# Kernel optimization log

Measured on AMD Instinct MI355X. Metric: run time of the kernel, lower is better.

## Reference

```python
import jax, jax.numpy as jnp
import numpy as np

B, T_ENC, D_IN = 64, 32, 4096
T_DEC, D_WORD = 20, 300
H = 512
VOCAB = 20000


def lstm_scan(x_tbd, W, b, c0, h0):
    """TF BasicLSTMCell (forget_bias=1.0, gate order i,j,f,o) scanned over time.
    x_tbd: [T,B,D]; W: [D+H, 4H]; returns (c,h) final state and all h [T,B,H]."""
    def step(carry, x):
        c, h = carry
        z = jnp.concatenate([x, h], axis=-1) @ W + b  # [B,4H]
        i, j, f, o = jnp.split(z, 4, axis=-1)
        c = c * jax.nn.sigmoid(f + 1.0) + jax.nn.sigmoid(i) * jnp.tanh(j)
        h = jnp.tanh(c) * jax.nn.sigmoid(o)
        return (c, h), h
    (c, h), hs = jax.lax.scan(step, (c0, h0), x_tbd)
    return (c, h), hs


def setup_inputs() -> dict:
    key = jax.random.key(0)
    ks = jax.random.split(key, 8)
    frames = jax.random.normal(ks[0], (B, T_ENC, D_IN), dtype=jnp.float32)
    caption = jax.random.randint(ks[1], (B, T_DEC), 0, VOCAB, dtype=jnp.int32)
    embeddings = jax.random.normal(ks[2], (VOCAB, D_WORD), dtype=jnp.float32) * 0.1
    s_enc = 1.0 / np.sqrt(D_IN + H)
    s_dec = 1.0 / np.sqrt(D_WORD + H)
    W_enc = jax.random.normal(ks[3], (D_IN + H, 4 * H), dtype=jnp.float32) * s_enc
    b_enc = jnp.zeros((4 * H,), dtype=jnp.float32)
    W_dec = jax.random.normal(ks[4], (D_WORD + H, 4 * H), dtype=jnp.float32) * s_dec
    b_dec = jnp.zeros((4 * H,), dtype=jnp.float32)
    W_proj = jax.random.normal(ks[5], (H, D_WORD), dtype=jnp.float32) / np.sqrt(H)
    b_proj = jnp.zeros((D_WORD,), dtype=jnp.float32)
    return {"frames": frames, "embeddings": embeddings, "W_enc": W_enc,
            "b_enc": b_enc, "W_dec": W_dec, "b_dec": b_dec,
            "W_proj": W_proj, "b_proj": b_proj, "caption": caption}


def reference(frames, embeddings, W_enc, b_enc, W_dec, b_dec, W_proj, b_proj, caption):
    b = frames.shape[0]
    c0 = jnp.zeros((b, H), dtype=frames.dtype)
    h0 = jnp.zeros((b, H), dtype=frames.dtype)
    # encoder over frames (dropout keep_prob=1 -> identity)
    (c, h), _ = lstm_scan(jnp.swapaxes(frames, 0, 1), W_enc, b_enc, c0, h0)
    # teacher-forced decoder over caption embeddings
    cap_emb = embeddings[caption]                      # [B,T_dec,D_word]
    _, hs = lstm_scan(jnp.swapaxes(cap_emb, 0, 1), W_dec, b_dec, c, h)  # [T,B,H]
    # per-step shared dense hidden->word, vectorized over time
    word_vecs = hs @ W_proj + b_proj                   # [T,B,D_word]
    return jnp.swapaxes(word_vecs, 0, 1)               # [B,T_dec,D_word]
```

## Files before the change

kernel.cpp:

```cpp
#include <hip/hip_runtime.h>
#include <hip/hip_bf16.h>

#define BATCH  64
#define T_ENC  32
#define D_IN   4096
#define T_DEC  20
#define D_WORD 300
#define HID    512
#define FOURH  2048
#define NWG    64
#define FPAD   32
#define ZP     13
#define CNT_BASE 2048
#define FLAGS_N  3520

typedef __attribute__((ext_vector_type(8))) short short8;
typedef __attribute__((ext_vector_type(4))) float f32x4;
typedef unsigned long long ull;

static __device__ __forceinline__ unsigned short f2bf(float f){
  union { float f; unsigned u; } v; v.f = f;
  unsigned r = v.u + 0x7fffu + ((v.u >> 16) & 1u);
  return (unsigned short)(r >> 16);
}
static __device__ __forceinline__ float bf2f(unsigned short b){
  union { unsigned u; float f; } v; v.u = ((unsigned)b) << 16;
  return v.f;
}
static __device__ __forceinline__ float sigm(float x){
  return __builtin_amdgcn_rcpf(1.f + __expf(-x));
}
static __device__ __forceinline__ float tanh_f(float x){
  float e = __expf(2.f * x);
  return 1.f - 2.f * __builtin_amdgcn_rcpf(e + 1.f);
}

__global__ __launch_bounds__(256) void prep(
    const float* __restrict__ frames, const float* __restrict__ W_enc,
    unsigned short* __restrict__ fb, unsigned short* __restrict__ wt,
    unsigned* __restrict__ flags, float* __restrict__ Xe)
{
  const int g = blockIdx.x * 256 + threadIdx.x;
  if (blockIdx.x == 0){
    for (int i = threadIdx.x; i < FLAGS_N; i += 256)
      __hip_atomic_store(&flags[i], 0u, __ATOMIC_RELAXED, __HIP_MEMORY_SCOPE_AGENT);
  }
  {
    float2 z2; z2.x = 0.f; z2.y = 0.f;
    *(float2*)(Xe + (long)g * 2) = z2;
  }
  if (g < 1048576){
    const long base = (long)g * 8;
    float4 x0 = *(const float4*)(frames + base);
    float4 x1 = *(const float4*)(frames + base + 4);
    short8 v;
    v[0] = (short)f2bf(x0.x); v[1] = (short)f2bf(x0.y);
    v[2] = (short)f2bf(x0.z); v[3] = (short)f2bf(x0.w);
    v[4] = (short)f2bf(x1.x); v[5] = (short)f2bf(x1.y);
    v[6] = (short)f2bf(x1.z); v[7] = (short)f2bf(x1.w);
    *(short8*)(fb + base) = v;
  } else {
    const int r  = g - 1048576;
    const int k0 = (r >> 11) << 3;
    const int c  = r & 2047;
    short8 v;
#pragma unroll
    for (int j = 0; j < 8; ++j)
      v[j] = (short)f2bf(W_enc[(long)(k0 + j) * FOURH + c]);
    *(short8*)&wt[(long)c * D_IN + k0] = v;
  }
}

__device__ __forceinline__ void enc_tile8(
    int bx, int by, int kc,
    const unsigned short* __restrict__ A0, const unsigned short* __restrict__ Wt,
    float* Z, char* smem, unsigned* flags)
{
  char* As = smem;
  char* Bs = smem + 16384;
  const int tid = threadIdx.x;
  const int row0 = bx * 128, col0 = by * 128;

  const int ar = tid >> 2, ah = tid & 3;
  long asrc;
  {
    int R = row0 + ar;
    int b = R & 63, t = R >> 6;
    asrc = (long)(b * T_ENC + t) * D_IN;
  }
  const int bc = tid & 127, bh = tid >> 7;
  const long bsrc = (long)(col0 + bc) * D_IN;
  const long kbase = (long)kc * 1024;

  const int wave = tid >> 6, lane = tid & 63;
  const int wm = (wave >> 2) * 64, wn = (wave & 3) * 32;
  const int lr = lane & 15, lkb = (lane >> 4) << 4, lq = (lane >> 4) << 2;

  f32x4 acc[4][2];
#pragma unroll
  for (int m = 0; m < 4; ++m)
#pragma unroll
    for (int n = 0; n < 2; ++n) acc[m][n] = (f32x4){0.f, 0.f, 0.f, 0.f};

#define ELOAD8(DA, DB, IT) do { \
    const long ka = kbase + (long)(IT) * 64 + ah * 16; \
    const long kb = kbase + (long)(IT) * 64 + bh * 16; \
    _Pragma("unroll") \
    for (int j = 0; j < 2; ++j){ \
      DA[j] = *(const short8*)(A0 + asrc + ka + j * 8); \
      DB[j] = *(const short8*)(Wt + bsrc + kb + j * 8); \
    } \
  } while (0)

  short8 aR[2], bR[2];
  ELOAD8(aR, bR, 0);

  for (int it = 0; it < 16; ++it){
    __syncthreads();
#pragma unroll
    for (int j = 0; j < 2; ++j){
      *(short8*)(As + ar * 128 + ((ah * 32 + j * 16) ^ ((ar & 7) << 4))) = aR[j];
      *(short8*)(Bs + bc * 128 + ((bh * 32 + j * 16) ^ ((bc & 7) << 4))) = bR[j];
    }
    __syncthreads();
    short8 aN[2], bN[2];
    if (it < 15) ELOAD8(aN, bN, it + 1);
#pragma unroll
    for (int kk = 0; kk < 2; ++kk){
      short8 af[4], bfv[2];
#pragma unroll
      for (int m = 0; m < 4; ++m){
        const int r = wm + m * 16 + lr;
        af[m] = *(const short8*)(As + r * 128 + ((kk * 64 + lkb) ^ ((r & 7) << 4)));
      }
#pragma unroll
      for (int n = 0; n < 2; ++n){
        const int r = wn + n * 16 + lr;
        bfv[n] = *(const short8*)(Bs + r * 128 + ((kk * 64 + lkb) ^ ((r & 7) << 4)));
      }
#pragma unroll
      for (int m = 0; m < 4; ++m)
#pragma unroll
        for (int n = 0; n < 2; ++n)
          acc[m][n] = __builtin_amdgcn_mfma_f32_16x16x32_bf16(af[m], bfv[n], acc[m][n], 0, 0, 0);
    }
    if (it < 15){
      aR[0] = aN[0]; aR[1] = aN[1]; bR[0] = bN[0]; bR[1] = bN[1];
    }
  }
#undef ELOAD8

#pragma unroll
  for (int m = 0; m < 4; ++m)
#pragma unroll
    for (int n = 0; n < 2; ++n)
#pragma unroll
      for (int r = 0; r < 4; ++r){
        int gr = row0 + wm + m * 16 + lq + r;
        int gc = col0 + wn + n * 16 + lr;
        __hip_atomic_fetch_add(&Z[(long)gr * FOURH + gc], acc[m][n][r],
                               __ATOMIC_RELAXED, __HIP_MEMORY_SCOPE_AGENT);
      }
  __syncthreads();
  if (tid == 0)
    __hip_atomic_fetch_add(&flags[CNT_BASE + bx * 32], 1u,
                           __ATOMIC_RELAXED, __HIP_MEMORY_SCOPE_AGENT);
}

__device__ __forceinline__ void dec_tile8(
    int bx, int by, const float* __restrict__ emb, const int* __restrict__ cap,
    const float* __restrict__ W, float* Z, char* smem, unsigned* flags)
{
  constexpr int KLIM  = D_WORD;
  constexpr int ITERS = (KLIM + 31) / 32;
  short* As = (short*)smem;
  short* Bs = (short*)(smem + 10240);
  const int tid = threadIdx.x;
  const int row0 = bx * 128, col0 = by * 128;

  const int ar = tid >> 2, akq = (tid & 3) * 8;
  long asrc;
  {
    int R = row0 + ar;
    int b = R & 63, t = R >> 6;
    asrc = (long)cap[b * T_DEC + t] * D_WORD;
  }
  const int bc = tid & 127, bkq = (tid >> 7) * 8;

  const int wave = tid >> 6, lane = tid & 63;
  const int wm = (wave >> 2) * 64, wn = (wave & 3) * 32;
  const int lr = lane & 15, lk = (lane >> 4) << 3, lq = (lane >> 4) << 2;

  f32x4 acc[4][2];
#pragma unroll
  for (int m = 0; m < 4; ++m)
#pragma unroll
    for (int n = 0; n < 2; ++n) acc[m][n] = (f32x4){0.f, 0.f, 0.f, 0.f};

  for (int it = 0; it < ITERS; ++it){
    const int k0 = it * 32;
    float av[8], bv[8];
#pragma unroll
    for (int i = 0; i < 8; ++i){
      int k = k0 + akq + i;
      av[i] = (k < KLIM) ? emb[asrc + k] : 0.f;
    }
#pragma unroll
    for (int i = 0; i < 8; ++i){
      int k = k0 + bkq + i;
      bv[i] = (k < KLIM) ? W[(long)k * FOURH + col0 + bc] : 0.f;
    }
    __syncthreads();
    short8 a8, b8;
#pragma unroll
    for (int i = 0; i < 8; ++i){
      a8[i] = (short)f2bf(av[i]);  b8[i] = (short)f2bf(bv[i]);
    }
    *(short8*)&As[ar * 40 + akq] = a8;
    *(short8*)&Bs[bc * 40 + bkq] = b8;
    __syncthreads();
    short8 af[4], bfv[2];
#pragma unroll
    for (int m = 0; m < 4; ++m) af[m]  = *(const short8*)&As[(wm + m * 16 + lr) * 40 + lk];
#pragma unroll
    for (int n = 0; n < 2; ++n) bfv[n] = *(const short8*)&Bs[(wn + n * 16 + lr) * 40 + lk];
#pragma unroll
    for (int m = 0; m < 4; ++m)
#pragma unroll
      for (int n = 0; n < 2; ++n)
        acc[m][n] = __builtin_amdgcn_mfma_f32_16x16x32_bf16(af[m], bfv[n], acc[m][n], 0, 0, 0);
  }

#pragma unroll
  for (int m = 0; m < 4; ++m)
#pragma unroll
    for (int n = 0; n < 2; ++n)
#pragma unroll
      for (int r = 0; r < 4; ++r){
        int gr = row0 + wm + m * 16 + lq + r;
        int gc = col0 + wn + n * 16 + lr;
        __hip_atomic_store(&Z[(long)gr * FOURH + gc], acc[m][n][r],
                           __ATOMIC_RELAXED, __HIP_MEMORY_SCOPE_AGENT);
      }
  __syncthreads();
  if (tid == 0)
    __hip_atomic_fetch_add(&flags[CNT_BASE + (16 + bx) * 32], 1u,
                           __ATOMIC_RELAXED, __HIP_MEMORY_SCOPE_AGENT);
}

__device__ __forceinline__ void proj_tail(
    int p, const unsigned short* __restrict__ hsd, const float* __restrict__ Wp,
    const float* __restrict__ bp, float* __restrict__ out,
    unsigned* flags, char* smem)
{
  float* hl = (float*)smem;
  const int tid = threadIdx.x;
  const int r0 = p * 16;
  const int t  = r0 >> 6;

  {
    unsigned* dc = &flags[CNT_BASE + (26 + t) * 32];
    while (__hip_atomic_load(dc, __ATOMIC_RELAXED, __HIP_MEMORY_SCOPE_AGENT) < 64u)
      __builtin_amdgcn_s_sleep(16);
  }
  __builtin_amdgcn_sched_barrier(0);

  for (int idx = tid; idx < 16 * 512; idx += 512)
    hl[idx] = bf2f(hsd[(long)r0 * 512 + idx]);
  __syncthreads();
  if (tid < D_WORD){
    const int d = tid;
    float acc[16];
#pragma unroll
    for (int r = 0; r < 16; ++r) acc[r] = bp[d];
    for (int k = 0; k < 512; ++k){
      float w = Wp[k * D_WORD + d];
#pragma unroll
      for (int r = 0; r < 16; ++r) acc[r] += hl[r * 512 + k] * w;
    }
#pragma unroll
    for (int r = 0; r < 16; ++r){
      int R = r0 + r;
      int tt = R >> 6, b = R & 63;
      out[(long)(b * T_DEC + tt) * D_WORD + d] = acc[r];
    }
  }
}

#define REC_GEMM(WREG) do { \
  _Pragma("unroll") \
  for (int kk = 0; kk < 8; ++kk){ \
    const int row = mh * 16 + lr; \
    short8 af = *(const short8*)(hlds + row * 1024 + \
                ((kh * 512 + kk * 64 + lkb) ^ ((row & 7) << 4))); \
    _Pragma("unroll") \
    for (int n = 0; n < 2; ++n) \
      acc[n] = __builtin_amdgcn_mfma_f32_16x16x32_bf16(af, WREG[kk][n], acc[n], 0, 0, 0); \
  } \
} while (0)

__global__ __launch_bounds__(512, 1) void fused(
    const unsigned short* __restrict__ fbf, const unsigned short* __restrict__ wbf,
    float* Xe,
    const float* __restrict__ emb, const int* __restrict__ cap,
    const float* __restrict__ W_dec, float* Xd,
    const float* __restrict__ Wre, const float* __restrict__ Wrd,
    const float* __restrict__ b_enc, const float* __restrict__ b_dec,
    const float* __restrict__ Wp, const float* __restrict__ bp,
    float* __restrict__ out,
    unsigned* hbuf_u, unsigned* hsd_u, unsigned* flags)
{
  __shared__ __align__(16) char smem[65536];
  const int bid = blockIdx.x;

  if (bid >= 64){
    int g = bid - 64;
    if (g < 512)        enc_tile8(g >> 6, g & 15, (g >> 4) & 3, fbf, wbf, Xe, smem, flags);
    else if (g < 672){  int d = g - 512; dec_tile8(d >> 4, d & 15, emb, cap, W_dec, Xd, smem, flags); }
    else if (g < 1184){ int e = g - 672; enc_tile8(8 + (e >> 6), e & 15, (e >> 4) & 3, fbf, wbf, Xe, smem, flags); }
    else                proj_tail(g - 1184, (const unsigned short*)hsd_u, Wp, bp, out, flags, smem);
    return;
  }

  __builtin_amdgcn_s_setprio(1);
  char*  hlds = smem;
  float* zlds = (float*)smem;
  const int tid = threadIdx.x, wgid = bid;
  const int wave = tid >> 6, lane = tid & 63;
  const int kh = wave >> 2, mh = wave & 3;
  const int lr = lane & 15, lk = (lane >> 4) << 3;
  const int lkb = (lane >> 4) << 4, lq = (lane >> 4) << 2;

  int ocol[2];
#pragma unroll
  for (int n = 0; n < 2; ++n)
    ocol[n] = (n * 2 + (lr >> 3)) * 512 + wgid * 8 + (lr & 7);

  short8 we[8][2], wd[8][2];
#pragma unroll
  for (int kk = 0; kk < 8; ++kk)
#pragma unroll
    for (int n = 0; n < 2; ++n){
      short8 e, d;
#pragma unroll
      for (int j = 0; j < 8; ++j){
        int k = kh * 256 + kk * 32 + lk + j;
        e[j] = (short)f2bf(Wre[(long)k * FOURH + ocol[n]]);
        d[j] = (short)f2bf(Wrd[(long)k * FOURH + ocol[n]]);
      }
      we[kk][n] = e; wd[kk][n] = d;
    }

  const int cb_ = tid >> 3, cu = tid & 7;
  float c_reg = 0.f;

  float be4[4], bd4[4];
#pragma unroll
  for (int gg = 0; gg < 4; ++gg){
    be4[gg] = b_enc[gg * 512 + wgid * 8 + cu];
    bd4[gg] = b_dec[gg * 512 + wgid * 8 + cu];
  }

  if (tid < 128)
    __hip_atomic_store((ull*)hbuf_u + ((tid >> 1) * 128 + wgid * 2 + (tid & 1)), 0ull,
                       __ATOMIC_RELAXED, __HIP_MEMORY_SCOPE_AGENT);
  __syncthreads();
  if (tid == 0)
    __hip_atomic_store(&flags[wgid * FPAD], 1u,
                       __ATOMIC_RELAXED, __HIP_MEMORY_SCOPE_AGENT);

  const bool mine = (lane != wgid);

  for (int q = 0; q < T_ENC + T_DEC; ++q){
    const bool dec = (q >= T_ENC);
    const int tt = dec ? q - T_ENC : q;
    float* Xp = dec ? Xd : Xe;

    if (!(tt & 1)){
      unsigned* xc = dec ? &flags[CNT_BASE + (16 + (tt >> 1)) * 32]
                         : &flags[CNT_BASE + (tt >> 1) * 32];
      const unsigned xtgt = dec ? 16u : 64u;
      while (__hip_atomic_load(xc, __ATOMIC_RELAXED, __HIP_MEMORY_SCOPE_AGENT) < xtgt)
        __builtin_amdgcn_s_sleep(2);
    }
    __builtin_amdgcn_sched_barrier(0);

    const long xb = (long)(tt * BATCH + cb_) * FOURH + wgid * 8 + cu;
    float xi = __hip_atomic_load(&Xp[xb],        __ATOMIC_RELAXED, __HIP_MEMORY_SCOPE_AGENT);
    float xj = __hip_atomic_load(&Xp[xb +  512], __ATOMIC_RELAXED, __HIP_MEMORY_SCOPE_AGENT);
    float xf = __hip_atomic_load(&Xp[xb + 1024], __ATOMIC_RELAXED, __HIP_MEMORY_SCOPE_AGENT);
    float xo = __hip_atomic_load(&Xp[xb + 1536], __ATOMIC_RELAXED, __HIP_MEMORY_SCOPE_AGENT);

    {
      const unsigned tgt = (unsigned)(q + 1);
      for (;;){
        unsigned f = tgt;
        if (mine) f = __hip_atomic_load(&flags[lane * FPAD],
                                        __ATOMIC_RELAXED, __HIP_MEMORY_SCOPE_AGENT);
        if (__all((int)(f >= tgt))) break;
        __builtin_amdgcn_s_sleep(1);
      }
    }
    __builtin_amdgcn_sched_barrier(0);

    const ull* rb8 = (const ull*)(hbuf_u + (q & 1) * (BATCH * HID / 2));
    ull hv[16];
#pragma unroll
    for (int j = 0; j < 16; ++j)
      hv[j] = __hip_atomic_load(rb8 + tid + j * 512,
                                __ATOMIC_RELAXED, __HIP_MEMORY_SCOPE_AGENT);
#pragma unroll
    for (int j = 0; j < 16; ++j){
      int idx8 = tid + j * 512;
      int row = idx8 >> 7, cbb = (idx8 & 127) << 3;
      *(ull*)(hlds + row * 1024 + (cbb ^ ((row & 7) << 4))) = hv[j];
    }
    __syncthreads();

    f32x4 acc[2];
#pragma unroll
    for (int n = 0; n < 2; ++n) acc[n] = (f32x4){0.f, 0.f, 0.f, 0.f};
    if (!dec) REC_GEMM(we); else REC_GEMM(wd);

    __syncthreads();

#pragma unroll
    for (int n = 0; n < 2; ++n){
      const int g = n * 2 + (lr >> 3), u = lr & 7;
#pragma unroll
      for (int r = 0; r < 4; ++r){
        const int row = mh * 16 + lq + r;
        zlds[((kh * 4 + g) * 64 + row) * ZP + u] = acc[n][r];
      }
    }
    __syncthreads();

    const int zb = cb_ * ZP + cu;
    float zi = zlds[(0 * 64) * ZP + zb] + zlds[(4 * 64) * ZP + zb] + xi + (dec ? bd4[0] : be4[0]);
    float zj = zlds[(1 * 64) * ZP + zb] + zlds[(5 * 64) * ZP + zb] + xj + (dec ? bd4[1] : be4[1]);
    float zf = zlds[(2 * 64) * ZP + zb] + zlds[(6 * 64) * ZP + zb] + xf + (dec ? bd4[2] : be4[2]);
    float zo = zlds[(3 * 64) * ZP + zb] + zlds[(7 * 64) * ZP + zb] + xo + (dec ? bd4[3] : be4[3]);
    c_reg = c_reg * sigm(zf + 1.f) + sigm(zi) * tanh_f(zj);
    float hn = tanh_f(c_reg) * sigm(zo);
    unsigned short hb = f2bf(hn);

    unsigned short* wb = (unsigned short*)(hbuf_u + ((q + 1) & 1) * (BATCH * HID / 2));
    __hip_atomic_store(&wb[cb_ * 512 + wgid * 8 + cu], hb,
                       __ATOMIC_RELAXED, __HIP_MEMORY_SCOPE_AGENT);
    if (dec)
      __hip_atomic_store(&((unsigned short*)hsd_u)[(tt * BATCH + cb_) * 512 + wgid * 8 + cu],
                         hb, __ATOMIC_RELAXED, __HIP_MEMORY_SCOPE_AGENT);

    __syncthreads();
    if (tid == 0)
      __hip_atomic_store(&flags[wgid * FPAD], (unsigned)(q + 2),
                         __ATOMIC_RELAXED, __HIP_MEMORY_SCOPE_AGENT);
    if (dec && tid == 64)
      __hip_atomic_fetch_add(&flags[CNT_BASE + (26 + tt) * 32], 1u,
                             __ATOMIC_RELAXED, __HIP_MEMORY_SCOPE_AGENT);
  }
}

extern "C" void kernel_launch(void* const* d_in, const int* in_sizes, int n_in,
                              void* d_out, int out_size, void* d_ws, size_t ws_size,
                              hipStream_t stream)
{
  const float* frames  = (const float*)d_in[0];
  const float* emb     = (const float*)d_in[1];
  const float* W_enc   = (const float*)d_in[2];
  const float* b_enc   = (const float*)d_in[3];
  const float* W_dec   = (const float*)d_in[4];
  const float* b_dec   = (const float*)d_in[5];
  const float* W_proj  = (const float*)d_in[6];
  const float* b_proj  = (const float*)d_in[7];
  const int*   caption = (const int*)d_in[8];

  char* ws = (char*)d_ws;
  float*          Xe    = (float*)(ws + 0);
  float*          Xd    = (float*)(ws + 16777216);
  unsigned*       hbuf  = (unsigned*)(ws + 27262976);
  unsigned*       hsd   = (unsigned*)(ws + 27394048);
  unsigned*       flags = (unsigned*)(ws + 28704768);
  unsigned short* fbf   = (unsigned short*)(ws + 28721152);
  unsigned short* wbf   = (unsigned short*)(ws + 45498368);
  float* out = (float*)d_out;

  prep<<<8192, 256, 0, stream>>>(frames, W_enc, fbf, wbf, flags, Xe);
  fused<<<64 + 1184 + 80, 512, 0, stream>>>(
      fbf, wbf, Xe, emb, caption, W_dec, Xd,
      W_enc + (long)D_IN * FOURH,
      W_dec + (long)D_WORD * FOURH,
      b_enc, b_dec, W_proj, b_proj, out,
      hbuf, hsd, flags);
}
```

Before: 306.6 us.

## Load recurrent h directly into MFMA A-fragments via an MFMA-friendly global layout

Changes the global hidden-state exchange buffer to a layout where each workgroup's 8 hidden units for all 64 batch rows are contiguous. Each wave then loads its bf16 A-operand fragments straight from global memory into registers. This removes the LDS staging of the full h matrix and one or two __syncthreads per recurrent step. Each wave now issues its own strided global loads of only the slices it needs, rather than a cooperative coalesced copy. The s_setprio raise is also narrowed to just the MFMA section.

Result: faster. 295.1 us (-3.7%).

```diff
diff --git a/kernel.cpp b/kernel.cpp
--- a/kernel.cpp
+++ b/kernel.cpp
@@ -290,9 +290,9 @@
 #define REC_GEMM(WREG) do { \
   _Pragma("unroll") \
   for (int kk = 0; kk < 8; ++kk){ \
-    const int row = mh * 16 + lr; \
-    short8 af = *(const short8*)(hlds + row * 1024 + \
-                ((kh * 512 + kk * 64 + lkb) ^ ((row & 7) << 4))); \
+    short8 af; \
+    ((ull*)&af)[0] = ha[2 * kk]; \
+    ((ull*)&af)[1] = ha[2 * kk + 1]; \
     _Pragma("unroll") \
     for (int n = 0; n < 2; ++n) \
       acc[n] = __builtin_amdgcn_mfma_f32_16x16x32_bf16(af, WREG[kk][n], acc[n], 0, 0, 0); \
@@ -322,14 +322,12 @@
     return;
   }
 
-  __builtin_amdgcn_s_setprio(1);
-  char*  hlds = smem;
   float* zlds = (float*)smem;
   const int tid = threadIdx.x, wgid = bid;
   const int wave = tid >> 6, lane = tid & 63;
   const int kh = wave >> 2, mh = wave & 3;
   const int lr = lane & 15, lk = (lane >> 4) << 3;
-  const int lkb = (lane >> 4) << 4, lq = (lane >> 4) << 2;
+  const int hi = lane >> 4, lq = (lane >> 4) << 2;
 
   int ocol[2];
 #pragma unroll
@@ -362,7 +360,7 @@
   }
 
   if (tid < 128)
-    __hip_atomic_store((ull*)hbuf_u + ((tid >> 1) * 128 + wgid * 2 + (tid & 1)), 0ull,
+    __hip_atomic_store((ull*)hbuf_u + wgid * 128 + tid, 0ull,
                        __ATOMIC_RELAXED, __HIP_MEMORY_SCOPE_AGENT);
   __syncthreads();
   if (tid == 0)
@@ -370,6 +368,7 @@
                        __ATOMIC_RELAXED, __HIP_MEMORY_SCOPE_AGENT);
 
   const bool mine = (lane != wgid);
+  const int b2 = (mh * 16 + lr) * 2;
 
   for (int q = 0; q < T_ENC + T_DEC; ++q){
     const bool dec = (q >= T_ENC);
@@ -403,26 +402,21 @@
     }
     __builtin_amdgcn_sched_barrier(0);
 
-    const ull* rb8 = (const ull*)(hbuf_u + (q & 1) * (BATCH * HID / 2));
-    ull hv[16];
-#pragma unroll
-    for (int j = 0; j < 16; ++j)
-      hv[j] = __hip_atomic_load(rb8 + tid + j * 512,
-                                __ATOMIC_RELAXED, __HIP_MEMORY_SCOPE_AGENT);
-#pragma unroll
-    for (int j = 0; j < 16; ++j){
-      int idx8 = tid + j * 512;
-      int row = idx8 >> 7, cbb = (idx8 & 127) << 3;
-      *(ull*)(hlds + row * 1024 + (cbb ^ ((row & 7) << 4))) = hv[j];
-    }
-    __syncthreads();
+    const ull* rb = (const ull*)hbuf_u + (q & 1) * 8192;
+    ull ha[16];
+#pragma unroll
+    for (int kk = 0; kk < 8; ++kk){
+      const int o = (kh * 32 + kk * 4 + hi) * 128 + b2;
+      ha[2 * kk]     = __hip_atomic_load(rb + o,     __ATOMIC_RELAXED, __HIP_MEMORY_SCOPE_AGENT);
+      ha[2 * kk + 1] = __hip_atomic_load(rb + o + 1, __ATOMIC_RELAXED, __HIP_MEMORY_SCOPE_AGENT);
+    }
 
     f32x4 acc[2];
 #pragma unroll
     for (int n = 0; n < 2; ++n) acc[n] = (f32x4){0.f, 0.f, 0.f, 0.f};
+    __builtin_amdgcn_s_setprio(1);
     if (!dec) REC_GEMM(we); else REC_GEMM(wd);
-
-    __syncthreads();
+    __builtin_amdgcn_s_setprio(0);
 
 #pragma unroll
     for (int n = 0; n < 2; ++n){
@@ -444,9 +438,8 @@
     float hn = tanh_f(c_reg) * sigm(zo);
     unsigned short hb = f2bf(hn);
 
-    unsigned short* wb = (unsigned short*)(hbuf_u + ((q + 1) & 1) * (BATCH * HID / 2));
-    __hip_atomic_store(&wb[cb_ * 512 + wgid * 8 + cu], hb,
-                       __ATOMIC_RELAXED, __HIP_MEMORY_SCOPE_AGENT);
+    __hip_atomic_store(&((unsigned short*)hbuf_u)[((q + 1) & 1) * 32768 + wgid * 512 + tid],
+                       hb, __ATOMIC_RELAXED, __HIP_MEMORY_SCOPE_AGENT);
     if (dec)
       __hip_atomic_store(&((unsigned short*)hsd_u)[(tt * BATCH + cb_) * 512 + wgid * 8 + cu],
                          hb, __ATOMIC_RELAXED, __HIP_MEMORY_SCOPE_AGENT);
```
